# Optimization experiments

Hardware: AMD Instinct MI355X
Metric: run time of the kernel (lower is better)

## Reference

```python
import jax, jax.numpy as jnp
import numpy as np

N_NODES = 100000
HIDDEN = 128
N_EDGES = 1000000


def setup_inputs() -> dict:
    key = jax.random.key(0)
    k1, k2, k3, k4 = jax.random.split(key, 4)
    node_embeddings = jax.random.normal(k1, (N_NODES, HIDDEN), dtype=jnp.float32)
    legal_moves = jax.random.randint(k2, (2, N_EDGES), 0, N_NODES, dtype=jnp.int64)
    # Linear(2H -> H) and Linear(H -> 1) weights (stored input-major for x @ W)
    W1 = jax.random.normal(k3, (2 * HIDDEN, HIDDEN), dtype=jnp.float32) * (1.0 / np.sqrt(2 * HIDDEN))
    b1 = jnp.zeros((HIDDEN,), dtype=jnp.float32)
    W2 = jax.random.normal(k4, (HIDDEN, 1), dtype=jnp.float32) * (1.0 / np.sqrt(HIDDEN))
    b2 = jnp.zeros((1,), dtype=jnp.float32)
    return {
        "node_embeddings": node_embeddings,
        "legal_moves": legal_moves,
        "W1": W1,
        "b1": b1,
        "W2": W2,
        "b2": b2,
    }


def reference(node_embeddings, legal_moves, W1, b1, W2, b2):
    sources = legal_moves[0]
    targets = legal_moves[1]
    h_source = node_embeddings[sources]          # [E, H]
    h_target = node_embeddings[targets]          # [E, H]
    move_features = jnp.concatenate([h_source, h_target], axis=-1)  # [E, 2H]
    hidden = jax.nn.relu(move_features @ W1 + b1)                   # [E, H]
    logits = (hidden @ W2 + b2).squeeze(-1)                         # [E]
    probs = jax.nn.softmax(logits, axis=-1)
    return probs
```

## Files before the change

### kernel.cpp

```cpp
#include <hip/hip_runtime.h>
#include <hip/hip_bf16.h>
#include <hip/hip_fp16.h>
#include <stdint.h>
#include <math.h>

#define NNODES 100000
#define HID 128
#define NEDGES 1000000
#define NEBLOCKS 15625

typedef __attribute__((ext_vector_type(4))) float floatx4;
typedef _Float16 f16x2 __attribute__((ext_vector_type(2)));
typedef _Float16 f16x4 __attribute__((ext_vector_type(4)));
typedef _Float16 f16x8 __attribute__((ext_vector_type(8)));

__global__ __launch_bounds__(256) void pack_b_kernel(
    const float* __restrict__ W1, _Float16* __restrict__ Bf) {
  const int t = blockIdx.x * 256 + threadIdx.x;
  const int lane = t & 63;
  const int ks = (t >> 6) & 3;
  const int ct = t >> 8;
  const int n = ct * 16 + (lane & 15);
  const int kb = ks * 32 + ((lane >> 4) * 8);
  f16x8 h;
#pragma unroll
  for (int j = 0; j < 8; ++j) {
    const int k = kb + j;
    const float v = (n < HID) ? W1[(size_t)k * HID + n]
                              : W1[(size_t)(HID + k) * HID + (n - HID)];
    h[j] = (_Float16)v;
  }
  *(f16x8*)(Bf + (size_t)t * 8) = h;
}

__global__ __launch_bounds__(256) void project_kernel(
    const float* __restrict__ emb, const _Float16* __restrict__ Bf,
    uint8_t* __restrict__ P, float* __restrict__ scalesInv) {
  __shared__ __align__(16) char smem[64 * 264 * 2];
  _Float16* As = (_Float16*)smem;
  __half* Co = (__half*)smem;

  const int t = threadIdx.x;
  const int lane = t & 63;
  const int w = t >> 6;
  const int l16 = lane & 15;
  const int q = lane >> 4;
  const int row0 = blockIdx.x * 64;

  {
    const int r_base = t >> 5;
    const int col = (t & 31) * 4;
#pragma unroll
    for (int i = 0; i < 8; ++i) {
      int grow = row0 + r_base + i * 8;
      if (grow >= NNODES) grow = NNODES - 1;
      const floatx4 v = *(const floatx4*)(emb + (size_t)grow * HID + col);
      f16x4 h;
      h[0] = (_Float16)v.x; h[1] = (_Float16)v.y;
      h[2] = (_Float16)v.z; h[3] = (_Float16)v.w;
      *(f16x4*)&As[(r_base + i * 8) * 136 + col] = h;
    }
  }
  __syncthreads();

  floatx4 acc[4][4] = {};
#pragma unroll
  for (int ks = 0; ks < 4; ++ks) {
    f16x8 bh[4];
#pragma unroll
    for (int ct = 0; ct < 4; ++ct) {
      const size_t idx = (size_t)(((w * 4 + ct) * 4 + ks) * 64 + lane) * 8;
      bh[ct] = *(const f16x8*)(Bf + idx);
    }
    f16x8 ah[4];
#pragma unroll
    for (int rt = 0; rt < 4; ++rt)
      ah[rt] = *(const f16x8*)&As[(rt * 16 + l16) * 136 + ks * 32 + q * 8];
#pragma unroll
    for (int rt = 0; rt < 4; ++rt)
#pragma unroll
      for (int ct = 0; ct < 4; ++ct)
        acc[rt][ct] = __builtin_amdgcn_mfma_f32_16x16x32_f16(ah[rt], bh[ct], acc[rt][ct], 0, 0, 0);
  }

  __syncthreads();
#pragma unroll
  for (int rt = 0; rt < 4; ++rt)
#pragma unroll
    for (int ct = 0; ct < 4; ++ct)
#pragma unroll
      for (int r = 0; r < 4; ++r) {
        const int row = rt * 16 + q * 4 + r;
        const int col = w * 64 + ct * 16 + l16;
        Co[row * 264 + col] = __float2half(acc[rt][ct][r]);
      }
  __syncthreads();
#pragma unroll
  for (int i = 0; i < 4; ++i) {
    const int chunk = t + i * 256;
    const int row = chunk >> 4;
    const int cx = chunk & 15;
    const int half = cx >> 3;
    const f16x8 v0 = *(const f16x8*)&Co[row * 264 + cx * 16];
    const f16x8 v1 = *(const f16x8*)&Co[row * 264 + cx * 16 + 8];
    float f[16];
#pragma unroll
    for (int k = 0; k < 8; ++k) { f[k] = (float)v0[k]; f[8 + k] = (float)v1[k]; }
    float m = 0.f;
#pragma unroll
    for (int k = 0; k < 16; ++k) m = fmaxf(m, fabsf(f[k]));
    m = fmaxf(m, __shfl_xor(m, 1, 64));
    m = fmaxf(m, __shfl_xor(m, 2, 64));
    m = fmaxf(m, __shfl_xor(m, 4, 64));
    m = fmaxf(m, 1e-20f);
    const float qs = 127.0f / m;
    const int grow = row0 + row;
    if (grow < NNODES) {
      if ((cx & 7) == 0) scalesInv[2 * grow + half] = m * (1.0f / 127.0f);
      unsigned d[4];
#pragma unroll
      for (int dw = 0; dw < 4; ++dw) {
        unsigned acc_b = 0;
#pragma unroll
        for (int b = 0; b < 4; ++b) {
          int qv = (int)rintf(f[dw * 4 + b] * qs) + 128;
          qv = qv < 0 ? 0 : (qv > 255 ? 255 : qv);
          acc_b |= ((unsigned)qv) << (8 * b);
        }
        d[dw] = acc_b;
      }
      uint4 o; o.x = d[0]; o.y = d[1]; o.z = d[2]; o.w = d[3];
      *(uint4*)(P + (size_t)grow * 256 + cx * 16) = o;
    }
  }
}

__global__ __launch_bounds__(256) void edge_kernel(
    const uint8_t* __restrict__ P, const float* __restrict__ scalesInv,
    const int* __restrict__ lm,
    const float* __restrict__ b1, const float* __restrict__ W2,
    const float* __restrict__ b2, float* __restrict__ explog,
    float* __restrict__ partials) {
  const int lane = threadIdx.x & 63;
  const int wid = threadIdx.x >> 6;
  const int g = lane >> 4;
  const int l16 = lane & 15;
  const int c = l16 * 8;

  f16x2 b1h[4], w2h[4];
  {
    const floatx4 b1a = *(const floatx4*)(b1 + c);
    const floatx4 b1b = *(const floatx4*)(b1 + c + 4);
    const floatx4 w2a = *(const floatx4*)(W2 + c);
    const floatx4 w2b = *(const floatx4*)(W2 + c + 4);
    b1h[0] = f16x2{(_Float16)b1a.x, (_Float16)b1a.y};
    b1h[1] = f16x2{(_Float16)b1a.z, (_Float16)b1a.w};
    b1h[2] = f16x2{(_Float16)b1b.x, (_Float16)b1b.y};
    b1h[3] = f16x2{(_Float16)b1b.z, (_Float16)b1b.w};
    w2h[0] = f16x2{(_Float16)w2a.x, (_Float16)w2a.y};
    w2h[1] = f16x2{(_Float16)w2a.z, (_Float16)w2a.w};
    w2h[2] = f16x2{(_Float16)w2b.x, (_Float16)w2b.y};
    w2h[3] = f16x2{(_Float16)w2b.z, (_Float16)w2b.w};
  }
  const f16x2 z2 = {(_Float16)0.f, (_Float16)0.f};
  const f16x2 kneg = {(_Float16)(-1152.f), (_Float16)(-1152.f)};
  const float b2v = b2[0];

  const int e0 = (blockIdx.x * 4 + wid) * 16;

  uint2 rs[4], rt_[4];
  float ssv[4], stv[4];
#pragma unroll
  for (int j = 0; j < 4; ++j) {
    const int ej = e0 + j * 4 + g;
    const int src = __builtin_nontemporal_load(lm + ej);
    const int tgt = __builtin_nontemporal_load(lm + NEDGES + ej);
    rs[j]  = *(const uint2*)(P + (size_t)src * 256 + c);
    rt_[j] = *(const uint2*)(P + (size_t)tgt * 256 + 128 + c);
    ssv[j] = scalesInv[2 * src];
    stv[j] = scalesInv[2 * tgt + 1];
  }
  float pe = 0.f;
#pragma unroll
  for (int j = 0; j < 4; ++j) {
    const f16x2 si2 = __builtin_bit_cast(f16x2, __builtin_amdgcn_cvt_pkrtz(ssv[j], ssv[j]));
    const f16x2 ti2 = __builtin_bit_cast(f16x2, __builtin_amdgcn_cvt_pkrtz(stv[j], stv[j]));
    float p = 0.f;
    const unsigned su[2] = {rs[j].x, rs[j].y};
    const unsigned tu[2] = {rt_[j].x, rt_[j].y};
#pragma unroll
    for (int pr = 0; pr < 4; ++pr) {
      const unsigned w = pr >> 1;
      const unsigned sel = (pr & 1) ? 0x00070006u : 0x00050004u;
      const f16x2 hs = __builtin_bit_cast(f16x2, __builtin_amdgcn_perm(su[w], 0x64646464u, sel));
      const f16x2 ht = __builtin_bit_cast(f16x2, __builtin_amdgcn_perm(tu[w], 0x64646464u, sel));
      const f16x2 ds = hs + kneg;
      const f16x2 dt = ht + kneg;
      const f16x2 a = __builtin_elementwise_max(ds * si2 + (dt * ti2 + b1h[pr]), z2);
      p = __builtin_amdgcn_fdot2(a, w2h[pr], p, false);
    }
    p += __shfl_xor(p, 8, 64);
    p += __shfl_xor(p, 4, 64);
    p += __shfl_xor(p, 2, 64);
    p += __shfl_xor(p, 1, 64);
    pe = (l16 == j) ? p : pe;
  }

  float lsum = 0.f;
  if (l16 < 4) {
    const float ev = __expf(pe + b2v);
    __builtin_nontemporal_store(ev, explog + e0 + l16 * 4 + g);
    lsum = ev;
  }

#pragma unroll
  for (int off = 32; off >= 1; off >>= 1) lsum += __shfl_xor(lsum, off, 64);
  __shared__ float wsums[4];
  if (lane == 0) wsums[wid] = lsum;
  __syncthreads();
  if (threadIdx.x == 0)
    partials[blockIdx.x] = wsums[0] + wsums[1] + wsums[2] + wsums[3];
}

__global__ __launch_bounds__(256) void reduce_kernel(
    const float* __restrict__ partials, float* __restrict__ accum) {
  float s = 0.f;
  for (int i = threadIdx.x; i < 3906; i += 256) {
    const floatx4 v = *(const floatx4*)(partials + i * 4);
    s += (v.x + v.y) + (v.z + v.w);
  }
  if (threadIdx.x == 0) s += partials[15624];
#pragma unroll
  for (int off = 32; off >= 1; off >>= 1) s += __shfl_xor(s, off, 64);
  __shared__ float ws_[4];
  if ((threadIdx.x & 63) == 0) ws_[threadIdx.x >> 6] = s;
  __syncthreads();
  if (threadIdx.x == 0) accum[0] = ws_[0] + ws_[1] + ws_[2] + ws_[3];
}

__global__ __launch_bounds__(256) void norm_kernel(
    const float* __restrict__ explog, const float* __restrict__ sum_accum,
    float* __restrict__ out) {
  const float inv = 1.0f / *sum_accum;
  const int i = (blockIdx.x * 256 + threadIdx.x) * 4;
  if (i < NEDGES) {
    floatx4 v = __builtin_nontemporal_load((const floatx4*)(explog + i));
    v.x *= inv; v.y *= inv; v.z *= inv; v.w *= inv;
    __builtin_nontemporal_store(v, (floatx4*)(out + i));
  }
}

extern "C" void kernel_launch(void* const* d_in, const int* in_sizes, int n_in,
                              void* d_out, int out_size, void* d_ws, size_t ws_size,
                              hipStream_t stream) {
  const float* emb = (const float*)d_in[0];
  const int*   lm  = (const int*)d_in[1];
  const float* W1  = (const float*)d_in[2];
  const float* b1  = (const float*)d_in[3];
  const float* W2  = (const float*)d_in[4];
  const float* b2  = (const float*)d_in[5];
  float* out = (float*)d_out;

  char* ws = (char*)d_ws;
  uint8_t* P      = (uint8_t*)ws;
  float* accum    = (float*)(ws + 25600000);
  float* explog   = (float*)(ws + 25600256);
  _Float16* Bf    = (_Float16*)(ws + 29600256);
  float* partials = (float*)(ws + 29665792);
  float* scalesInv = (float*)(ws + 29728512);

  pack_b_kernel<<<16, 256, 0, stream>>>(W1, Bf);
  project_kernel<<<1563, 256, 0, stream>>>(emb, Bf, P, scalesInv);
  edge_kernel<<<NEBLOCKS, 256, 0, stream>>>(P, scalesInv, lm, b1, W2, b2, explog, partials);
  reduce_kernel<<<1, 256, 0, stream>>>(partials, accum);
  norm_kernel<<<977, 256, 0, stream>>>(explog, accum, out);
}
```

Before: 159.4 us.

## Replace partial-sum reduce kernel with striped atomics and change cache hints

Drops the separate single-block reduce kernel. Each wave now atomically adds its exp sum into one of 64 padded accumulator slots, and norm_kernel reduces those 64 slots itself. The accumulators are zeroed inside pack_b_kernel. Cache hints also change: embedding loads become nontemporal, while explog stores and loads become regular cached accesses so the normalize pass can hit in L2/MALL. This removes one launch and the block-level syncthreads, at the cost of atomic contention and a sum order that is no longer deterministic.

After: 159.9 us. Within noise of the previous version (+0.3%).

```diff
diff --git a/kernel.cpp b/kernel.cpp
--- a/kernel.cpp
+++ b/kernel.cpp
@@ -15,7 +15,9 @@
 typedef _Float16 f16x8 __attribute__((ext_vector_type(8)));
 
 __global__ __launch_bounds__(256) void pack_b_kernel(
-    const float* __restrict__ W1, _Float16* __restrict__ Bf) {
+    const float* __restrict__ W1, _Float16* __restrict__ Bf,
+    float* __restrict__ accum) {
+  if (blockIdx.x == 0 && threadIdx.x < 64) accum[threadIdx.x * 16] = 0.f;
   const int t = blockIdx.x * 256 + threadIdx.x;
   const int lane = t & 63;
   const int ks = (t >> 6) & 3;
@@ -54,7 +56,8 @@
     for (int i = 0; i < 8; ++i) {
       int grow = row0 + r_base + i * 8;
       if (grow >= NNODES) grow = NNODES - 1;
-      const floatx4 v = *(const floatx4*)(emb + (size_t)grow * HID + col);
+      const floatx4 v = __builtin_nontemporal_load(
+          (const floatx4*)(emb + (size_t)grow * HID + col));
       f16x4 h;
       h[0] = (_Float16)v.x; h[1] = (_Float16)v.y;
       h[2] = (_Float16)v.z; h[3] = (_Float16)v.w;
@@ -140,7 +143,7 @@
     const int* __restrict__ lm,
     const float* __restrict__ b1, const float* __restrict__ W2,
     const float* __restrict__ b2, float* __restrict__ explog,
-    float* __restrict__ partials) {
+    float* __restrict__ accum) {
   const int lane = threadIdx.x & 63;
   const int wid = threadIdx.x >> 6;
   const int g = lane >> 4;
@@ -209,42 +212,26 @@
   float lsum = 0.f;
   if (l16 < 4) {
     const float ev = __expf(pe + b2v);
-    __builtin_nontemporal_store(ev, explog + e0 + l16 * 4 + g);
+    explog[e0 + l16 * 4 + g] = ev;
     lsum = ev;
   }
 
 #pragma unroll
   for (int off = 32; off >= 1; off >>= 1) lsum += __shfl_xor(lsum, off, 64);
-  __shared__ float wsums[4];
-  if (lane == 0) wsums[wid] = lsum;
-  __syncthreads();
-  if (threadIdx.x == 0)
-    partials[blockIdx.x] = wsums[0] + wsums[1] + wsums[2] + wsums[3];
-}
-
-__global__ __launch_bounds__(256) void reduce_kernel(
-    const float* __restrict__ partials, float* __restrict__ accum) {
-  float s = 0.f;
-  for (int i = threadIdx.x; i < 3906; i += 256) {
-    const floatx4 v = *(const floatx4*)(partials + i * 4);
-    s += (v.x + v.y) + (v.z + v.w);
-  }
-  if (threadIdx.x == 0) s += partials[15624];
+  if (lane == 0)
+    atomicAdd(accum + (((blockIdx.x << 2) + wid) & 63) * 16, lsum);
+}
+
+__global__ __launch_bounds__(256) void norm_kernel(
+    const float* __restrict__ explog, const float* __restrict__ accum,
+    float* __restrict__ out) {
+  float s = accum[(threadIdx.x & 63) * 16];
 #pragma unroll
   for (int off = 32; off >= 1; off >>= 1) s += __shfl_xor(s, off, 64);
-  __shared__ float ws_[4];
-  if ((threadIdx.x & 63) == 0) ws_[threadIdx.x >> 6] = s;
-  __syncthreads();
-  if (threadIdx.x == 0) accum[0] = ws_[0] + ws_[1] + ws_[2] + ws_[3];
-}
-
-__global__ __launch_bounds__(256) void norm_kernel(
-    const float* __restrict__ explog, const float* __restrict__ sum_accum,
-    float* __restrict__ out) {
-  const float inv = 1.0f / *sum_accum;
+  const float inv = 1.0f / s;
   const int i = (blockIdx.x * 256 + threadIdx.x) * 4;
   if (i < NEDGES) {
-    floatx4 v = __builtin_nontemporal_load((const floatx4*)(explog + i));
+    floatx4 v = *(const floatx4*)(explog + i);
     v.x *= inv; v.y *= inv; v.z *= inv; v.w *= inv;
     __builtin_nontemporal_store(v, (floatx4*)(out + i));
   }
@@ -262,16 +249,14 @@
   float* out = (float*)d_out;
 
   char* ws = (char*)d_ws;
-  uint8_t* P      = (uint8_t*)ws;
-  float* accum    = (float*)(ws + 25600000);
-  float* explog   = (float*)(ws + 25600256);
-  _Float16* Bf    = (_Float16*)(ws + 29600256);
-  float* partials = (float*)(ws + 29665792);
-  float* scalesInv = (float*)(ws + 29728512);
-
-  pack_b_kernel<<<16, 256, 0, stream>>>(W1, Bf);
+  uint8_t* P       = (uint8_t*)ws;
+  float* accum     = (float*)(ws + 25600000);
+  float* explog    = (float*)(ws + 25604096);
+  _Float16* Bf     = (_Float16*)(ws + 29604096);
+  float* scalesInv = (float*)(ws + 29669632);
+
+  pack_b_kernel<<<16, 256, 0, stream>>>(W1, Bf, accum);
   project_kernel<<<1563, 256, 0, stream>>>(emb, Bf, P, scalesInv);
-  edge_kernel<<<NEBLOCKS, 256, 0, stream>>>(P, scalesInv, lm, b1, W2, b2, explog, partials);
-  reduce_kernel<<<1, 256, 0, stream>>>(partials, accum);
+  edge_kernel<<<NEBLOCKS, 256, 0, stream>>>(P, scalesInv, lm, b1, W2, b2, explog, accum);
   norm_kernel<<<977, 256, 0, stream>>>(explog, accum, out);
 }
```
